# Kernel tuning notes

Measured on AMD Instinct MI355X. Metric: run time of the kernel, lower is better.

The kernel has to match this reference:

```python
import jax, jax.numpy as jnp
import numpy as np

VOCAB, EMBD, H1, H2, OUT = 100000, 128, 256, 128, 1
EPS = 1e-12

def _layernorm(x, g, b):
    mu = jnp.mean(x, axis=-1, keepdims=True)
    var = jnp.mean(jnp.square(x - mu), axis=-1, keepdims=True)
    return (x - mu) * jax.lax.rsqrt(var + EPS) * g + b

def setup_inputs() -> dict:
    key = jax.random.key(0)
    ks = jax.random.split(key, 10)
    B, S = 4096, 50
    return {
        "entity_ids": jax.random.randint(ks[0], (B, S), 0, VOCAB),
        "entity_length": jax.random.randint(ks[1], (B,), 0, S + 1),
        "emb_table": jax.random.normal(ks[2], (VOCAB, EMBD), jnp.float32),
        "ln1_g": jnp.ones((EMBD,), jnp.float32),
        "ln1_b": jnp.zeros((EMBD,), jnp.float32),
        "w1": jax.random.normal(ks[3], (EMBD, H1), jnp.float32) * (1.0 / np.sqrt(EMBD)),
        "b1": jnp.zeros((H1,), jnp.float32),
        "w2": jax.random.normal(ks[4], (H1, H2), jnp.float32) * (1.0 / np.sqrt(H1)),
        "b2": jnp.zeros((H2,), jnp.float32),
        "ln2_g": jnp.ones((H2,), jnp.float32),
        "ln2_b": jnp.zeros((H2,), jnp.float32),
        "fc_w": jax.random.normal(ks[5], (H2, OUT), jnp.float32) * (1.0 / np.sqrt(H2)),
        "fc_b": jnp.zeros((OUT,), jnp.float32),
    }

def reference(entity_ids, entity_length, emb_table, ln1_g, ln1_b, w1, b1, w2, b2, ln2_g, ln2_b, fc_w, fc_b):
    # embed: [B, S, EMBD]
    x = emb_table[entity_ids]
    x = _layernorm(x, ln1_g, ln1_b)
    # MLP (dropout is identity in eval); torch GELU default is exact erf form
    x = jax.nn.gelu(x @ w1 + b1, approximate=False) @ w2 + b2  # [B, S, H2]
    # ragged max-pool over first length positions (length 0 treated as 1)
    lengths = jnp.maximum(entity_length, 1)  # [B]
    S = x.shape[1]
    mask = jnp.arange(S)[None, :] < lengths[:, None]  # [B, S]
    x = jnp.max(jnp.where(mask[:, :, None], x, -jnp.inf), axis=1)  # [B, H2]
    x = _layernorm(x, ln2_g, ln2_b)
    return (x @ fc_w + fc_b).squeeze(-1)  # [B]
```

## Files before the change

kernel.cpp:

```cpp
#include <hip/hip_runtime.h>
#include <hip/hip_bf16.h>
#include <math.h>

typedef __attribute__((ext_vector_type(8))) _Float16 half8;
typedef __attribute__((ext_vector_type(4))) float f32x4;

#define EMBD 128
#define H1 256
#define H2 128
#define SLEN 50
#define NR 4

__device__ __forceinline__ float gelu_exact(float h) {
    float ah = fabsf(h);
    float d  = fmaf(0.23163845f, ah, 1.0f);
    float t;
    asm("v_rcp_f32 %0, %1" : "=v"(t) : "v"(d));
    float p = fmaf(1.061405429f, t, -1.453152027f);
    p = fmaf(p, t, 1.421413741f);
    p = fmaf(p, t, -0.284496736f);
    p = fmaf(p, t, 0.254829592f);
    p = p * t;
    float e;
    float x2 = h * h * -0.72134752f;
    asm("v_exp_f32 %0, %1" : "=v"(e) : "v"(x2));
    float er = fmaf(-p, e, 1.0f);
    return fmaf(0.5f * ah, er, 0.5f * h);
}

#define BARRIER_LDS() asm volatile("s_waitcnt lgkmcnt(0)\n\ts_barrier" ::: "memory")

__global__ __launch_bounds__(256) void prep_weights(
    const float* __restrict__ w1, const float* __restrict__ w2,
    half8* __restrict__ ws)
{
    int f = blockIdx.x * 256 + threadIdx.x;
    half8 v;
    if (f < 4096) {
        int lane = f & 63;
        int nt = (f >> 6) & 3, kt = (f >> 8) & 3, w = (f >> 10) & 3;
        int col = w * 64 + nt * 16 + (lane & 15);
        int kb  = kt * 32 + (lane >> 4) * 8;
        #pragma unroll
        for (int i = 0; i < 8; ++i) v[i] = (_Float16)w1[(size_t)(kb + i) * H1 + col];
        ws[f] = v;
    } else {
        int f2 = f - 4096;
        int lane = f2 & 63;
        int nt = (f2 >> 6) & 1, kt = (f2 >> 7) & 7, w = (f2 >> 10) & 3;
        int col = w * 32 + nt * 16 + (lane & 15);
        int kb  = kt * 32 + (lane >> 4) * 8;
        #pragma unroll
        for (int i = 0; i < 8; ++i) v[i] = (_Float16)w2[(size_t)(kb + i) * H2 + col];
        ws[4096 + f2] = v;
    }
}

__global__ __launch_bounds__(256) void entity_encoder_kernel(
    const int* __restrict__ ids, const int* __restrict__ lens,
    const float* __restrict__ emb, const float* __restrict__ ln1g,
    const float* __restrict__ ln1b, const float* __restrict__ b1,
    const float* __restrict__ b2, const float* __restrict__ ln2g,
    const float* __restrict__ ln2b, const float* __restrict__ fcw,
    const float* __restrict__ fcb, const half8* __restrict__ wfrag,
    float* __restrict__ out)
{
    const int tid = threadIdx.x;
    const int w  = tid >> 6;
    const int l  = tid & 63;
    const int ln = l & 15;
    const int lg = l >> 4;

    __shared__ __align__(16) _Float16 x_lds[16][EMBD + 8];
    __shared__ __align__(16) _Float16 h1_lds[16][H1 + 8];
    __shared__ float pool_lds[H2];

    half8 w1f[4][4];
    #pragma unroll
    for (int kt = 0; kt < 4; ++kt)
      #pragma unroll
      for (int nt = 0; nt < 4; ++nt)
        w1f[kt][nt] = wfrag[((w * 4 + kt) * 4 + nt) * 64 + l];
    half8 w2f[8][2];
    #pragma unroll
    for (int kt = 0; kt < 8; ++kt)
      #pragma unroll
      for (int nt = 0; nt < 2; ++nt)
        w2f[kt][nt] = wfrag[4096 + ((w * 8 + kt) * 2 + nt) * 64 + l];

    float g1r[8], b1r[8];
    #pragma unroll
    for (int i = 0; i < 8; ++i) { g1r[i] = ln1g[ln * 8 + i]; b1r[i] = ln1b[ln * 8 + i]; }
    float b1v[4];
    #pragma unroll
    for (int nt = 0; nt < 4; ++nt) b1v[nt] = b1[w * 64 + nt * 16 + ln];
    float b2v[2];
    #pragma unroll
    for (int nt = 0; nt < 2; ++nt) b2v[nt] = b2[w * 32 + nt * 16 + ln];
    float g2a = ln2g[l], g2c = ln2g[l + 64];
    float b2a = ln2b[l], b2c = ln2b[l + 64];
    float fwa = fcw[l],  fwc = fcw[l + 64];
    float fcb0 = fcb[0];

    const int stride = gridDim.x;
    const int tok = w * 4 + lg;

    int rows[NR], Ts[NR];
    #pragma unroll
    for (int i = 0; i < NR; ++i) {
        rows[i] = blockIdx.x + i * stride;
        int T = lens[rows[i]];
        Ts[i] = T < 1 ? 1 : (T > SLEN ? SLEN : T);
    }

    float4 pa0, pa1; bool va;
    {
        va = (tok < Ts[0]);
        if (va) {
            int id = ids[rows[0] * SLEN + tok];
            const float4* src = (const float4*)(emb + (size_t)id * EMBD + ln * 8);
            pa0 = src[0]; pa1 = src[1];
        }
    }

    for (int i = 0; i < NR; ++i) {
        const int r = rows[i];
        const int T = Ts[i];
        const int ntiles = (T + 15) >> 4;
        float pool0 = -INFINITY, pool1 = -INFINITY;

        for (int mt = 0; mt < ntiles; ++mt) {
            half8 xo;
            if (va) {
                float v[8] = {pa0.x, pa0.y, pa0.z, pa0.w, pa1.x, pa1.y, pa1.z, pa1.w};
                float s = 0.f, ss = 0.f;
                #pragma unroll
                for (int k = 0; k < 8; ++k) { s += v[k]; ss += v[k] * v[k]; }
                #pragma unroll
                for (int m = 1; m < 16; m <<= 1) {
                    s  += __shfl_xor(s,  m, 64);
                    ss += __shfl_xor(ss, m, 64);
                }
                float mu  = s * (1.f / 128.f);
                float var = ss * (1.f / 128.f) - mu * mu;
                float rs  = rsqrtf(var + 1e-12f);
                #pragma unroll
                for (int k = 0; k < 8; ++k)
                    xo[k] = (_Float16)((v[k] - mu) * rs * g1r[k] + b1r[k]);
            } else {
                #pragma unroll
                for (int k = 0; k < 8; ++k) xo[k] = (_Float16)0.f;
            }
            *(half8*)&x_lds[tok][ln * 8] = xo;

            float4 pb0, pb1; bool vb = false;
            {
                int ni = i, nmt = mt + 1;
                if (nmt >= ntiles) { ni = i + 1; nmt = 0; }
                if (ni < NR) {
                    int tn = nmt * 16 + tok;
                    if (tn < Ts[ni]) {
                        vb = true;
                        int id = ids[rows[ni] * SLEN + tn];
                        const float4* src = (const float4*)(emb + (size_t)id * EMBD + ln * 8);
                        pb0 = src[0]; pb1 = src[1];
                    }
                }
            }

            BARRIER_LDS();

            f32x4 acc[4] = {{0,0,0,0},{0,0,0,0},{0,0,0,0},{0,0,0,0}};
            #pragma unroll
            for (int kt = 0; kt < 4; ++kt) {
                half8 a = *(const half8*)&x_lds[ln][kt * 32 + lg * 8];
                #pragma unroll
                for (int nt = 0; nt < 4; ++nt)
                    acc[nt] = __builtin_amdgcn_mfma_f32_16x16x32_f16(a, w1f[kt][nt], acc[nt], 0, 0, 0);
            }
            #pragma unroll
            for (int nt = 0; nt < 4; ++nt) {
                int col = w * 64 + nt * 16 + ln;
                #pragma unroll
                for (int g2 = 0; g2 < 4; ++g2) {
                    int row = lg * 4 + g2;
                    float h = acc[nt][g2] + b1v[nt];
                    h1_lds[row][col] = (_Float16)gelu_exact(h);
                }
            }

            BARRIER_LDS();

            f32x4 acc2[2] = {{0,0,0,0},{0,0,0,0}};
            #pragma unroll
            for (int kt = 0; kt < 8; ++kt) {
                half8 a = *(const half8*)&h1_lds[ln][kt * 32 + lg * 8];
                #pragma unroll
                for (int nt = 0; nt < 2; ++nt)
                    acc2[nt] = __builtin_amdgcn_mfma_f32_16x16x32_f16(a, w2f[kt][nt], acc2[nt], 0, 0, 0);
            }
            {
                float tm0 = -INFINITY, tm1 = -INFINITY;
                #pragma unroll
                for (int g2 = 0; g2 < 4; ++g2) {
                    int trow = lg * 4 + g2;
                    bool valid = (mt * 16 + trow) < T;
                    float h0  = acc2[0][g2] + b2v[0];
                    float h1v = acc2[1][g2] + b2v[1];
                    if (valid) { tm0 = fmaxf(tm0, h0); tm1 = fmaxf(tm1, h1v); }
                }
                tm0 = fmaxf(tm0, __shfl_xor(tm0, 16, 64));
                tm0 = fmaxf(tm0, __shfl_xor(tm0, 32, 64));
                tm1 = fmaxf(tm1, __shfl_xor(tm1, 16, 64));
                tm1 = fmaxf(tm1, __shfl_xor(tm1, 32, 64));
                pool0 = fmaxf(pool0, tm0);
                pool1 = fmaxf(pool1, tm1);
            }

            if (vb) { pa0 = pb0; pa1 = pb1; }
            va = vb;
        }

        if (l < 16) {
            pool_lds[w * 32 + ln]      = pool0;
            pool_lds[w * 32 + 16 + ln] = pool1;
        }
        BARRIER_LDS();

        float v0 = pool_lds[l], v1 = pool_lds[l + 64];
        float s = v0 + v1, ss = v0 * v0 + v1 * v1;
        #pragma unroll
        for (int m = 1; m < 64; m <<= 1) {
            s  += __shfl_xor(s,  m, 64);
            ss += __shfl_xor(ss, m, 64);
        }
        float mu  = s * (1.f / 128.f);
        float var = ss * (1.f / 128.f) - mu * mu;
        float rs  = rsqrtf(var + 1e-12f);
        float n0 = (v0 - mu) * rs * g2a + b2a;
        float n1 = (v1 - mu) * rs * g2c + b2c;
        float dot = n0 * fwa + n1 * fwc;
        #pragma unroll
        for (int m = 1; m < 64; m <<= 1) dot += __shfl_xor(dot, m, 64);
        if (tid == 0) out[r] = dot + fcb0;

        BARRIER_LDS();
    }
}

extern "C" void kernel_launch(void* const* d_in, const int* in_sizes, int n_in,
                              void* d_out, int out_size, void* d_ws, size_t ws_size,
                              hipStream_t stream) {
    const int*   ids  = (const int*)d_in[0];
    const int*   lens = (const int*)d_in[1];
    const float* emb  = (const float*)d_in[2];
    const float* ln1g = (const float*)d_in[3];
    const float* ln1b = (const float*)d_in[4];
    const float* w1   = (const float*)d_in[5];
    const float* b1   = (const float*)d_in[6];
    const float* w2   = (const float*)d_in[7];
    const float* b2   = (const float*)d_in[8];
    const float* ln2g = (const float*)d_in[9];
    const float* ln2b = (const float*)d_in[10];
    const float* fcw  = (const float*)d_in[11];
    const float* fcb  = (const float*)d_in[12];
    float* out = (float*)d_out;
    half8* ws = (half8*)d_ws;

    hipLaunchKernelGGL(prep_weights, dim3(32), dim3(256), 0, stream, w1, w2, ws);

    int nblocks = out_size / NR;
    hipLaunchKernelGGL(entity_encoder_kernel, dim3(nblocks), dim3(256), 0, stream,
                       ids, lens, emb, ln1g, ln1b, b1, b2, ln2g, ln2b, fcw, fcb,
                       ws, out);
}
```

Before: 69.85 us.

## Process two entity rows per tile pass to double MFMA M-dimension per barrier

```diff
diff --git a/kernel.cpp b/kernel.cpp
--- a/kernel.cpp
+++ b/kernel.cpp
@@ -9,7 +9,6 @@
 #define H1 256
 #define H2 128
 #define SLEN 50
-#define NR 4
 
 __device__ __forceinline__ float gelu_exact(float h) {
     float ah = fabsf(h);
@@ -56,7 +55,7 @@
     }
 }
 
-__global__ __launch_bounds__(256) void entity_encoder_kernel(
+__global__ __launch_bounds__(256, 2) void entity_encoder_kernel(
     const int* __restrict__ ids, const int* __restrict__ lens,
     const float* __restrict__ emb, const float* __restrict__ ln1g,
     const float* __restrict__ ln1b, const float* __restrict__ b1,
@@ -70,10 +69,11 @@
     const int l  = tid & 63;
     const int ln = l & 15;
     const int lg = l >> 4;
-
-    __shared__ __align__(16) _Float16 x_lds[16][EMBD + 8];
-    __shared__ __align__(16) _Float16 h1_lds[16][H1 + 8];
-    __shared__ float pool_lds[H2];
+    const int g16 = w * 4 + lg;
+
+    __shared__ __align__(16) _Float16 x_lds[32][EMBD + 8];
+    __shared__ __align__(16) _Float16 h1_lds[32][H1 + 8];
+    __shared__ float pool_lds[2][H2];
 
     half8 w1f[4][4];
     #pragma unroll
@@ -102,148 +102,177 @@
     float fwa = fcw[l],  fwc = fcw[l + 64];
     float fcb0 = fcb[0];
 
-    const int stride = gridDim.x;
-    const int tok = w * 4 + lg;
-
-    int rows[NR], Ts[NR];
-    #pragma unroll
-    for (int i = 0; i < NR; ++i) {
-        rows[i] = blockIdx.x + i * stride;
+    int rows[4], Ts[4];
+    #pragma unroll
+    for (int i = 0; i < 4; ++i) {
+        rows[i] = blockIdx.x + i * (int)gridDim.x;
         int T = lens[rows[i]];
         Ts[i] = T < 1 ? 1 : (T > SLEN ? SLEN : T);
     }
 
-    float4 pa0, pa1; bool va;
-    {
-        va = (tok < Ts[0]);
-        if (va) {
-            int id = ids[rows[0] * SLEN + tok];
+    float4 pa0[2], pa1[2]; bool va[2];
+    #pragma unroll
+    for (int s = 0; s < 2; ++s) {
+        va[s] = (g16 < Ts[s]);
+        if (va[s]) {
+            int id = ids[rows[s] * SLEN + g16];
             const float4* src = (const float4*)(emb + (size_t)id * EMBD + ln * 8);
-            pa0 = src[0]; pa1 = src[1];
+            pa0[s] = src[0]; pa1[s] = src[1];
         }
     }
 
-    for (int i = 0; i < NR; ++i) {
-        const int r = rows[i];
-        const int T = Ts[i];
-        const int ntiles = (T + 15) >> 4;
-        float pool0 = -INFINITY, pool1 = -INFINITY;
+    for (int j = 0; j < 2; ++j) {
+        const int TA = Ts[2 * j], TB = Ts[2 * j + 1];
+        const int ntA = (TA + 15) >> 4, ntB = (TB + 15) >> 4;
+        const int ntiles = ntA > ntB ? ntA : ntB;
+        float poolr[2][2];
+        #pragma unroll
+        for (int m = 0; m < 2; ++m) { poolr[m][0] = -INFINITY; poolr[m][1] = -INFINITY; }
 
         for (int mt = 0; mt < ntiles; ++mt) {
-            half8 xo;
-            if (va) {
-                float v[8] = {pa0.x, pa0.y, pa0.z, pa0.w, pa1.x, pa1.y, pa1.z, pa1.w};
-                float s = 0.f, ss = 0.f;
+            #pragma unroll
+            for (int s = 0; s < 2; ++s) {
+                half8 xo;
+                if (va[s]) {
+                    float v[8] = {pa0[s].x, pa0[s].y, pa0[s].z, pa0[s].w,
+                                  pa1[s].x, pa1[s].y, pa1[s].z, pa1[s].w};
+                    float sm = 0.f, ss = 0.f;
+                    #pragma unroll
+                    for (int k = 0; k < 8; ++k) { sm += v[k]; ss += v[k] * v[k]; }
+                    #pragma unroll
+                    for (int m = 1; m < 16; m <<= 1) {
+                        sm += __shfl_xor(sm, m, 64);
+                        ss += __shfl_xor(ss, m, 64);
+                    }
+                    float mu  = sm * (1.f / 128.f);
+                    float var = ss * (1.f / 128.f) - mu * mu;
+                    float rs  = rsqrtf(var + 1e-12f);
+                    #pragma unroll
+                    for (int k = 0; k < 8; ++k)
+                        xo[k] = (_Float16)((v[k] - mu) * rs * g1r[k] + b1r[k]);
+                } else {
+                    #pragma unroll
+                    for (int k = 0; k < 8; ++k) xo[k] = (_Float16)0.f;
+                }
+                *(half8*)&x_lds[s * 16 + g16][ln * 8] = xo;
+            }
+
+            float4 pb0[2], pb1[2]; bool vb[2] = {false, false};
+            {
+                int nj = j, nmt = mt + 1;
+                if (nmt >= ntiles) { nj = j + 1; nmt = 0; }
+                if (nj < 2) {
+                    #pragma unroll
+                    for (int s = 0; s < 2; ++s) {
+                        int tn = nmt * 16 + g16;
+                        if (tn < Ts[2 * nj + s]) {
+                            vb[s] = true;
+                            int id = ids[rows[2 * nj + s] * SLEN + tn];
+                            const float4* src = (const float4*)(emb + (size_t)id * EMBD + ln * 8);
+                            pb0[s] = src[0]; pb1[s] = src[1];
+                        }
+                    }
+                }
+            }
+
+            BARRIER_LDS();
+
+            f32x4 acc[2][4];
+            #pragma unroll
+            for (int m = 0; m < 2; ++m)
+              #pragma unroll
+              for (int nt = 0; nt < 4; ++nt) acc[m][nt] = (f32x4){0,0,0,0};
+            #pragma unroll
+            for (int kt = 0; kt < 4; ++kt) {
+                half8 a0 = *(const half8*)&x_lds[ln][kt * 32 + lg * 8];
+                half8 a1 = *(const half8*)&x_lds[16 + ln][kt * 32 + lg * 8];
                 #pragma unroll
-                for (int k = 0; k < 8; ++k) { s += v[k]; ss += v[k] * v[k]; }
-                #pragma unroll
-                for (int m = 1; m < 16; m <<= 1) {
-                    s  += __shfl_xor(s,  m, 64);
-                    ss += __shfl_xor(ss, m, 64);
-                }
-                float mu  = s * (1.f / 128.f);
-                float var = ss * (1.f / 128.f) - mu * mu;
-                float rs  = rsqrtf(var + 1e-12f);
-                #pragma unroll
-                for (int k = 0; k < 8; ++k)
-                    xo[k] = (_Float16)((v[k] - mu) * rs * g1r[k] + b1r[k]);
-            } else {
-                #pragma unroll
-                for (int k = 0; k < 8; ++k) xo[k] = (_Float16)0.f;
-            }
-            *(half8*)&x_lds[tok][ln * 8] = xo;
-
-            float4 pb0, pb1; bool vb = false;
-            {
-                int ni = i, nmt = mt + 1;
-                if (nmt >= ntiles) { ni = i + 1; nmt = 0; }
-                if (ni < NR) {
-                    int tn = nmt * 16 + tok;
-                    if (tn < Ts[ni]) {
-                        vb = true;
-                        int id = ids[rows[ni] * SLEN + tn];
-                        const float4* src = (const float4*)(emb + (size_t)id * EMBD + ln * 8);
-                        pb0 = src[0]; pb1 = src[1];
-                    }
-                }
-            }
-
-            BARRIER_LDS();
-
-            f32x4 acc[4] = {{0,0,0,0},{0,0,0,0},{0,0,0,0},{0,0,0,0}};
-            #pragma unroll
-            for (int kt = 0; kt < 4; ++kt) {
-                half8 a = *(const half8*)&x_lds[ln][kt * 32 + lg * 8];
-                #pragma unroll
-                for (int nt = 0; nt < 4; ++nt)
-                    acc[nt] = __builtin_amdgcn_mfma_f32_16x16x32_f16(a, w1f[kt][nt], acc[nt], 0, 0, 0);
-            }
-            #pragma unroll
-            for (int nt = 0; nt < 4; ++nt) {
+                for (int nt = 0; nt < 4; ++nt) {
+                    acc[0][nt] = __builtin_amdgcn_mfma_f32_16x16x32_f16(a0, w1f[kt][nt], acc[0][nt], 0, 0, 0);
+                    acc[1][nt] = __builtin_amdgcn_mfma_f32_16x16x32_f16(a1, w1f[kt][nt], acc[1][nt], 0, 0, 0);
+                }
+            }
+            #pragma unroll
+            for (int m = 0; m < 2; ++m)
+              #pragma unroll
+              for (int nt = 0; nt < 4; ++nt) {
                 int col = w * 64 + nt * 16 + ln;
                 #pragma unroll
                 for (int g2 = 0; g2 < 4; ++g2) {
-                    int row = lg * 4 + g2;
-                    float h = acc[nt][g2] + b1v[nt];
+                    int row = m * 16 + lg * 4 + g2;
+                    float h = acc[m][nt][g2] + b1v[nt];
                     h1_lds[row][col] = (_Float16)gelu_exact(h);
                 }
-            }
+              }
 
             BARRIER_LDS();
 
-            f32x4 acc2[2] = {{0,0,0,0},{0,0,0,0}};
+            f32x4 acc2[2][2];
+            #pragma unroll
+            for (int m = 0; m < 2; ++m) { acc2[m][0] = (f32x4){0,0,0,0}; acc2[m][1] = (f32x4){0,0,0,0}; }
             #pragma unroll
             for (int kt = 0; kt < 8; ++kt) {
-                half8 a = *(const half8*)&h1_lds[ln][kt * 32 + lg * 8];
+                half8 a0 = *(const half8*)&h1_lds[ln][kt * 32 + lg * 8];
+                half8 a1 = *(const half8*)&h1_lds[16 + ln][kt * 32 + lg * 8];
                 #pragma unroll
-                for (int nt = 0; nt < 2; ++nt)
-                    acc2[nt] = __builtin_amdgcn_mfma_f32_16x16x32_f16(a, w2f[kt][nt], acc2[nt], 0, 0, 0);
-            }
-            {
-                float tm0 = -INFINITY, tm1 = -INFINITY;
+                for (int nt = 0; nt < 2; ++nt) {
+                    acc2[0][nt] = __builtin_amdgcn_mfma_f32_16x16x32_f16(a0, w2f[kt][nt], acc2[0][nt], 0, 0, 0);
+                    acc2[1][nt] = __builtin_amdgcn_mfma_f32_16x16x32_f16(a1, w2f[kt][nt], acc2[1][nt], 0, 0, 0);
+                }
+            }
+            #pragma unroll
+            for (int m = 0; m < 2; ++m) {
+                const int Tm = m ? TB : TA;
                 #pragma unroll
-                for (int g2 = 0; g2 < 4; ++g2) {
-                    int trow = lg * 4 + g2;
-                    bool valid = (mt * 16 + trow) < T;
-                    float h0  = acc2[0][g2] + b2v[0];
-                    float h1v = acc2[1][g2] + b2v[1];
-                    if (valid) { tm0 = fmaxf(tm0, h0); tm1 = fmaxf(tm1, h1v); }
-                }
-                tm0 = fmaxf(tm0, __shfl_xor(tm0, 16, 64));
-                tm0 = fmaxf(tm0, __shfl_xor(tm0, 32, 64));
-                tm1 = fmaxf(tm1, __shfl_xor(tm1, 16, 64));
-                tm1 = fmaxf(tm1, __shfl_xor(tm1, 32, 64));
-                pool0 = fmaxf(pool0, tm0);
-                pool1 = fmaxf(pool1, tm1);
-            }
-
-            if (vb) { pa0 = pb0; pa1 = pb1; }
-            va = vb;
+                for (int nt = 0; nt < 2; ++nt) {
+                    float tm = -INFINITY;
+                    #pragma unroll
+                    for (int g2 = 0; g2 < 4; ++g2) {
+                        int trow = lg * 4 + g2;
+                        bool valid = (mt * 16 + trow) < Tm;
+                        float h = acc2[m][nt][g2] + b2v[nt];
+                        if (valid) tm = fmaxf(tm, h);
+                    }
+                    tm = fmaxf(tm, __shfl_xor(tm, 16, 64));
+                    tm = fmaxf(tm, __shfl_xor(tm, 32, 64));
+                    poolr[m][nt] = fmaxf(poolr[m][nt], tm);
+                }
+            }
+
+            #pragma unroll
+            for (int s = 0; s < 2; ++s) {
+                if (vb[s]) { pa0[s] = pb0[s]; pa1[s] = pb1[s]; }
+                va[s] = vb[s];
+            }
         }
 
-        if (l < 16) {
-            pool_lds[w * 32 + ln]      = pool0;
-            pool_lds[w * 32 + 16 + ln] = pool1;
+        if (lg == 0) {
+            #pragma unroll
+            for (int m = 0; m < 2; ++m)
+              #pragma unroll
+              for (int nt = 0; nt < 2; ++nt)
+                pool_lds[m][w * 32 + nt * 16 + ln] = poolr[m][nt];
         }
         BARRIER_LDS();
 
-        float v0 = pool_lds[l], v1 = pool_lds[l + 64];
-        float s = v0 + v1, ss = v0 * v0 + v1 * v1;
-        #pragma unroll
-        for (int m = 1; m < 64; m <<= 1) {
-            s  += __shfl_xor(s,  m, 64);
-            ss += __shfl_xor(ss, m, 64);
+        if (w < 2) {
+            float v0 = pool_lds[w][l], v1 = pool_lds[w][l + 64];
+            float s = v0 + v1, ss = v0 * v0 + v1 * v1;
+            #pragma unroll
+            for (int m = 1; m < 64; m <<= 1) {
+                s  += __shfl_xor(s,  m, 64);
+                ss += __shfl_xor(ss, m, 64);
+            }
+            float mu  = s * (1.f / 128.f);
+            float var = ss * (1.f / 128.f) - mu * mu;
+            float rs  = rsqrtf(var + 1e-12f);
+            float n0 = (v0 - mu) * rs * g2a + b2a;
+            float n1 = (v1 - mu) * rs * g2c + b2c;
+            float dot = n0 * fwa + n1 * fwc;
+            #pragma unroll
+            for (int m = 1; m < 64; m <<= 1) dot += __shfl_xor(dot, m, 64);
+            if (l == 0) out[rows[2 * j + w]] = dot + fcb0;
         }
-        float mu  = s * (1.f / 128.f);
-        float var = ss * (1.f / 128.f) - mu * mu;
-        float rs  = rsqrtf(var + 1e-12f);
-        float n0 = (v0 - mu) * rs * g2a + b2a;
-        float n1 = (v1 - mu) * rs * g2c + b2c;
-        float dot = n0 * fwa + n1 * fwc;
-        #pragma unroll
-        for (int m = 1; m < 64; m <<= 1) dot += __shfl_xor(dot, m, 64);
-        if (tid == 0) out[r] = dot + fcb0;
-
         BARRIER_LDS();
     }
 }
@@ -269,7 +298,7 @@
 
     hipLaunchKernelGGL(prep_weights, dim3(32), dim3(256), 0, stream, w1, w2, ws);
 
-    int nblocks = out_size / NR;
+    int nblocks = out_size / 4;
     hipLaunchKernelGGL(entity_encoder_kernel, dim3(nblocks), dim3(256), 0, stream,
                        ids, lens, emb, ln1g, ln1b, b1, b2, ln2g, ln2b, fcw, fcb,
                        ws, out);
```

After: 79.86 us. 14.3% more time.

## Double-buffer LDS tiles and swap MFMA operands for vectorized h1 stores

Applied to the files above, without the earlier changes.

```diff
diff --git a/kernel.cpp b/kernel.cpp
--- a/kernel.cpp
+++ b/kernel.cpp
@@ -3,6 +3,7 @@
 #include <math.h>
 
 typedef __attribute__((ext_vector_type(8))) _Float16 half8;
+typedef __attribute__((ext_vector_type(4))) _Float16 half4;
 typedef __attribute__((ext_vector_type(4))) float f32x4;
 
 #define EMBD 128
@@ -70,17 +71,18 @@
     const int l  = tid & 63;
     const int ln = l & 15;
     const int lg = l >> 4;
-
-    __shared__ __align__(16) _Float16 x_lds[16][EMBD + 8];
-    __shared__ __align__(16) _Float16 h1_lds[16][H1 + 8];
+    const int g16 = w * 4 + lg;
+
+    __shared__ __align__(16) _Float16 x_lds[2][16][EMBD + 8];
+    __shared__ __align__(16) _Float16 h1_lds[2][16][H1 + 8];
     __shared__ float pool_lds[H2];
 
     half8 w1f[4][4];
     #pragma unroll
     for (int kt = 0; kt < 4; ++kt)
       #pragma unroll
-      for (int nt = 0; nt < 4; ++nt)
-        w1f[kt][nt] = wfrag[((w * 4 + kt) * 4 + nt) * 64 + l];
+      for (int mt = 0; mt < 4; ++mt)
+        w1f[kt][mt] = wfrag[((w * 4 + kt) * 4 + mt) * 64 + l];
     half8 w2f[8][2];
     #pragma unroll
     for (int kt = 0; kt < 8; ++kt)
@@ -91,9 +93,10 @@
     float g1r[8], b1r[8];
     #pragma unroll
     for (int i = 0; i < 8; ++i) { g1r[i] = ln1g[ln * 8 + i]; b1r[i] = ln1b[ln * 8 + i]; }
-    float b1v[4];
-    #pragma unroll
-    for (int nt = 0; nt < 4; ++nt) b1v[nt] = b1[w * 64 + nt * 16 + ln];
+    f32x4 b1tv[4];
+    #pragma unroll
+    for (int mt = 0; mt < 4; ++mt)
+        b1tv[mt] = *(const f32x4*)&b1[w * 64 + mt * 16 + lg * 4];
     float b2v[2];
     #pragma unroll
     for (int nt = 0; nt < 2; ++nt) b2v[nt] = b2[w * 32 + nt * 16 + ln];
@@ -102,91 +105,126 @@
     float fwa = fcw[l],  fwc = fcw[l + 64];
     float fcb0 = fcb[0];
 
-    const int stride = gridDim.x;
-    const int tok = w * 4 + lg;
-
     int rows[NR], Ts[NR];
     #pragma unroll
     for (int i = 0; i < NR; ++i) {
-        rows[i] = blockIdx.x + i * stride;
+        rows[i] = blockIdx.x + i * (int)gridDim.x;
         int T = lens[rows[i]];
         Ts[i] = T < 1 ? 1 : (T > SLEN ? SLEN : T);
     }
 
     float4 pa0, pa1; bool va;
+    va = (g16 < Ts[0]);
+    if (va) {
+        int id = ids[rows[0] * SLEN + g16];
+        const float4* src = (const float4*)(emb + (size_t)id * EMBD + ln * 8);
+        pa0 = src[0]; pa1 = src[1];
+    }
     {
-        va = (tok < Ts[0]);
+        half8 xo;
         if (va) {
-            int id = ids[rows[0] * SLEN + tok];
+            float v[8] = {pa0.x, pa0.y, pa0.z, pa0.w, pa1.x, pa1.y, pa1.z, pa1.w};
+            float s = 0.f, ss = 0.f;
+            #pragma unroll
+            for (int k = 0; k < 8; ++k) { s += v[k]; ss += v[k] * v[k]; }
+            #pragma unroll
+            for (int m = 1; m < 16; m <<= 1) {
+                s  += __shfl_xor(s,  m, 64);
+                ss += __shfl_xor(ss, m, 64);
+            }
+            float mu  = s * (1.f / 128.f);
+            float var = ss * (1.f / 128.f) - mu * mu;
+            float rs  = rsqrtf(var + 1e-12f);
+            #pragma unroll
+            for (int k = 0; k < 8; ++k)
+                xo[k] = (_Float16)((v[k] - mu) * rs * g1r[k] + b1r[k]);
+        } else {
+            #pragma unroll
+            for (int k = 0; k < 8; ++k) xo[k] = (_Float16)0.f;
+        }
+        *(half8*)&x_lds[0][g16][ln * 8] = xo;
+    }
+    int i1 = 0, t1 = 1;
+    if (t1 >= ((Ts[0] + 15) >> 4)) { i1 = 1; t1 = 0; }
+    va = false;
+    if (i1 < NR) {
+        int tn = t1 * 16 + g16;
+        if (tn < Ts[i1]) {
+            va = true;
+            int id = ids[rows[i1] * SLEN + tn];
             const float4* src = (const float4*)(emb + (size_t)id * EMBD + ln * 8);
             pa0 = src[0]; pa1 = src[1];
         }
     }
+    BARRIER_LDS();
+    int cur = 0;
 
     for (int i = 0; i < NR; ++i) {
-        const int r = rows[i];
         const int T = Ts[i];
         const int ntiles = (T + 15) >> 4;
         float pool0 = -INFINITY, pool1 = -INFINITY;
 
-        for (int mt = 0; mt < ntiles; ++mt) {
-            half8 xo;
-            if (va) {
-                float v[8] = {pa0.x, pa0.y, pa0.z, pa0.w, pa1.x, pa1.y, pa1.z, pa1.w};
-                float s = 0.f, ss = 0.f;
-                #pragma unroll
-                for (int k = 0; k < 8; ++k) { s += v[k]; ss += v[k] * v[k]; }
-                #pragma unroll
-                for (int m = 1; m < 16; m <<= 1) {
-                    s  += __shfl_xor(s,  m, 64);
-                    ss += __shfl_xor(ss, m, 64);
-                }
-                float mu  = s * (1.f / 128.f);
-                float var = ss * (1.f / 128.f) - mu * mu;
-                float rs  = rsqrtf(var + 1e-12f);
-                #pragma unroll
-                for (int k = 0; k < 8; ++k)
-                    xo[k] = (_Float16)((v[k] - mu) * rs * g1r[k] + b1r[k]);
-            } else {
-                #pragma unroll
-                for (int k = 0; k < 8; ++k) xo[k] = (_Float16)0.f;
-            }
-            *(half8*)&x_lds[tok][ln * 8] = xo;
-
+        for (int t = 0; t < ntiles; ++t) {
+            int i2 = i1, t2 = t1;
             float4 pb0, pb1; bool vb = false;
-            {
-                int ni = i, nmt = mt + 1;
-                if (nmt >= ntiles) { ni = i + 1; nmt = 0; }
-                if (ni < NR) {
-                    int tn = nmt * 16 + tok;
-                    if (tn < Ts[ni]) {
+            if (i1 < NR) {
+                t2 = t1 + 1;
+                if (t2 >= ((Ts[i1] + 15) >> 4)) { i2 = i1 + 1; t2 = 0; }
+                if (i2 < NR) {
+                    int tn = t2 * 16 + g16;
+                    if (tn < Ts[i2]) {
                         vb = true;
-                        int id = ids[rows[ni] * SLEN + tn];
+                        int id = ids[rows[i2] * SLEN + tn];
                         const float4* src = (const float4*)(emb + (size_t)id * EMBD + ln * 8);
                         pb0 = src[0]; pb1 = src[1];
                     }
                 }
             }
 
-            BARRIER_LDS();
-
+            const _Float16* xb = &x_lds[cur][0][0];
+            _Float16*       hb = &h1_lds[cur][0][0];
             f32x4 acc[4] = {{0,0,0,0},{0,0,0,0},{0,0,0,0},{0,0,0,0}};
             #pragma unroll
             for (int kt = 0; kt < 4; ++kt) {
-                half8 a = *(const half8*)&x_lds[ln][kt * 32 + lg * 8];
+                half8 bfrag = *(const half8*)(xb + ln * (EMBD + 8) + kt * 32 + lg * 8);
                 #pragma unroll
-                for (int nt = 0; nt < 4; ++nt)
-                    acc[nt] = __builtin_amdgcn_mfma_f32_16x16x32_f16(a, w1f[kt][nt], acc[nt], 0, 0, 0);
-            }
-            #pragma unroll
-            for (int nt = 0; nt < 4; ++nt) {
-                int col = w * 64 + nt * 16 + ln;
+                for (int mt = 0; mt < 4; ++mt)
+                    acc[mt] = __builtin_amdgcn_mfma_f32_16x16x32_f16(w1f[kt][mt], bfrag, acc[mt], 0, 0, 0);
+            }
+            #pragma unroll
+            for (int mt = 0; mt < 4; ++mt) {
+                half4 hv;
                 #pragma unroll
                 for (int g2 = 0; g2 < 4; ++g2) {
-                    int row = lg * 4 + g2;
-                    float h = acc[nt][g2] + b1v[nt];
-                    h1_lds[row][col] = (_Float16)gelu_exact(h);
+                    float h = acc[mt][g2] + b1tv[mt][g2];
+                    hv[g2] = (_Float16)gelu_exact(h);
                 }
+                *(half4*)(hb + ln * (H1 + 8) + w * 64 + mt * 16 + lg * 4) = hv;
+            }
+
+            if (i1 < NR) {
+                half8 xo;
+                if (va) {
+                    float v[8] = {pa0.x, pa0.y, pa0.z, pa0.w, pa1.x, pa1.y, pa1.z, pa1.w};
+                    float s = 0.f, ss = 0.f;
+                    #pragma unroll
+                    for (int k = 0; k < 8; ++k) { s += v[k]; ss += v[k] * v[k]; }
+                    #pragma unroll
+                    for (int m = 1; m < 16; m <<= 1) {
+                        s  += __shfl_xor(s,  m, 64);
+                        ss += __shfl_xor(ss, m, 64);
+                    }
+                    float mu  = s * (1.f / 128.f);
+                    float var = ss * (1.f / 128.f) - mu * mu;
+                    float rs  = rsqrtf(var + 1e-12f);
+                    #pragma unroll
+                    for (int k = 0; k < 8; ++k)
+                        xo[k] = (_Float16)((v[k] - mu) * rs * g1r[k] + b1r[k]);
+                } else {
+                    #pragma unroll
+                    for (int k = 0; k < 8; ++k) xo[k] = (_Float16)0.f;
+                }
+                *(half8*)&x_lds[cur ^ 1][g16][ln * 8] = xo;
             }
 
             BARRIER_LDS();
@@ -194,7 +232,7 @@
             f32x4 acc2[2] = {{0,0,0,0},{0,0,0,0}};
             #pragma unroll
             for (int kt = 0; kt < 8; ++kt) {
-                half8 a = *(const half8*)&h1_lds[ln][kt * 32 + lg * 8];
+                half8 a = *(const half8*)(hb + ln * (H1 + 8) + kt * 32 + lg * 8);
                 #pragma unroll
                 for (int nt = 0; nt < 2; ++nt)
                     acc2[nt] = __builtin_amdgcn_mfma_f32_16x16x32_f16(a, w2f[kt][nt], acc2[nt], 0, 0, 0);
@@ -204,7 +242,7 @@
                 #pragma unroll
                 for (int g2 = 0; g2 < 4; ++g2) {
                     int trow = lg * 4 + g2;
-                    bool valid = (mt * 16 + trow) < T;
+                    bool valid = (t * 16 + trow) < T;
                     float h0  = acc2[0][g2] + b2v[0];
                     float h1v = acc2[1][g2] + b2v[1];
                     if (valid) { tm0 = fmaxf(tm0, h0); tm1 = fmaxf(tm1, h1v); }
@@ -218,7 +256,8 @@
             }
 
             if (vb) { pa0 = pb0; pa1 = pb1; }
-            va = vb;
+            va = vb; i1 = i2; t1 = t2;
+            cur ^= 1;
         }
 
         if (l < 16) {
@@ -242,7 +281,7 @@
         float dot = n0 * fwa + n1 * fwc;
         #pragma unroll
         for (int m = 1; m < 64; m <<= 1) dot += __shfl_xor(dot, m, 64);
-        if (tid == 0) out[r] = dot + fcb0;
+        if (tid == 0) out[rows[i]] = dot + fcb0;
 
         BARRIER_LDS();
     }
```

Result: faster. 68.05 us (-2.6%).
